# Optimization experiments

Measured on AMD Instinct MI355X. Metric: run time of the kernel, lower is better.

The kernel has to match this reference:

```python
import jax, jax.numpy as jnp
import numpy as np
from jax import lax

EPS = 1e-5
K = 3
PAD = 1
N_LAYERS = 7


def _conv2d(x, w, b):
    # x: [B,Cin,H,W], w: [Cout,Cin,K,K] -> [B,Cout,H,W], padding=1, stride=1
    y = lax.conv_general_dilated(x, w, window_strides=(1, 1),
                                 padding=[(PAD, PAD), (PAD, PAD)],
                                 dimension_numbers=('NCHW', 'OIHW', 'NCHW'))
    return y + b[None, :, None, None]


def _deform_conv2d(x, offset, weight):
    # torchvision deform_conv2d v1 (no mask, no bias), padding=PAD, stride=1.
    B, Cin, H, W = x.shape
    Cout = weight.shape[0]
    KK = K * K
    off = offset.reshape(B, KK, 2, H, W)
    dy = off[:, :, 0]  # [B,KK,H,W]
    dx = off[:, :, 1]
    kh = (jnp.arange(KK) // K).astype(x.dtype)  # row-major kernel taps
    kw = (jnp.arange(KK) % K).astype(x.dtype)
    hg = jnp.arange(H, dtype=x.dtype)
    wg = jnp.arange(W, dtype=x.dtype)
    # sampling positions p = p0 - pad + pk + offset
    py = dy + (hg[:, None] - PAD)[None, None, :, :] + kh[None, :, None, None]
    px = dx + (wg[None, :] - PAD)[None, None, :, :] + kw[None, :, None, None]
    y0 = jnp.floor(py)
    x0 = jnp.floor(px)
    ly = py - y0
    lx = px - x0
    y0i = y0.astype(jnp.int32)
    x0i = x0.astype(jnp.int32)

    def gather(img, yy, xx):  # img [Cin,H,W], yy/xx [KK,H,W]
        return img[:, yy, xx]  # [Cin,KK,H,W]

    gather_b = jax.vmap(gather)

    def corner(yi, xi, wgt):
        valid = (yi >= 0) & (yi < H) & (xi >= 0) & (xi < W)
        yc = jnp.clip(yi, 0, H - 1)
        xc = jnp.clip(xi, 0, W - 1)
        vals = gather_b(x, yc, xc)  # [B,Cin,KK,H,W]
        return vals * (wgt * valid)[:, None]

    sampled = (corner(y0i, x0i, (1 - ly) * (1 - lx))
               + corner(y0i, x0i + 1, (1 - ly) * lx)
               + corner(y0i + 1, x0i, ly * (1 - lx))
               + corner(y0i + 1, x0i + 1, ly * lx))  # [B,Cin,KK,H,W]
    return jnp.einsum('bikhw,oik->bohw', sampled, weight.reshape(Cout, Cin, KK))


def _layer(x, ow, ob, dw, g, b):
    offset = _conv2d(x, ow, ob)
    y = _deform_conv2d(x, offset, dw)
    # BatchNorm2d, training mode (batch stats, biased variance)
    mean = y.mean(axis=(0, 2, 3))
    var = y.var(axis=(0, 2, 3))
    yn = (y - mean[None, :, None, None]) * lax.rsqrt(var + EPS)[None, :, None, None]
    return jax.nn.relu(g[None, :, None, None] * yn + b[None, :, None, None])


def setup_inputs() -> dict:
    key = jax.random.key(0)
    ks = jax.random.split(key, 4)
    B, C, H, W = 4, 64, 128, 128
    x = jax.random.normal(ks[0], (B, C, H, W), dtype=jnp.float32)
    offset_w = jax.random.normal(ks[1], (N_LAYERS, 2 * K * K, C, K, K), dtype=jnp.float32) * 0.02
    offset_b = jnp.zeros((N_LAYERS, 2 * K * K), dtype=jnp.float32)
    deform_w = jax.random.normal(ks[2], (N_LAYERS, C, C, K, K), dtype=jnp.float32) * 0.05
    gamma = jnp.ones((N_LAYERS, C), dtype=jnp.float32)
    beta = jnp.zeros((N_LAYERS, C), dtype=jnp.float32)
    return {"x": x, "offset_w": offset_w, "offset_b": offset_b,
            "deform_w": deform_w, "gamma": gamma, "beta": beta}


def reference(x, offset_w, offset_b, deform_w, gamma, beta):
    def L(i, t):
        return _layer(t, offset_w[i], offset_b[i], deform_w[i], gamma[i], beta[i])
    # layer index map: 0=1_1, 1=1_2, 2=1_3, 3=1_4, 4=2_1, 5=2_2, 6=3
    out_1 = L(1, L(0, x))
    out_2 = L(4, x)
    out_sum_1 = out_1 + out_2
    out_1 = L(3, L(2, out_sum_1))
    out_2 = L(5, out_sum_1)
    out_3 = L(6, out_sum_1)
    return out_1 + out_2 + out_3
```

## Files before the change

### kernel.cpp

```cpp
#include <hip/hip_runtime.h>
#include <hip/hip_bf16.h>
#include <hip/hip_fp16.h>

#define NTOT 4194304
typedef __attribute__((ext_vector_type(4)))  short short4v;
typedef __attribute__((ext_vector_type(8)))  short short8v;
typedef __attribute__((ext_vector_type(4)))  float f32x4;
typedef __attribute__((ext_vector_type(2)))  float fx2;
typedef __attribute__((ext_vector_type(4)))  unsigned int uint4v;

__device__ __forceinline__ ushort f2bf(float f){
    __hip_bfloat16 h = __float2bfloat16(f);
    return __bfloat16_as_ushort(h);
}
__device__ __forceinline__ float bf2f(ushort u){
    return __uint_as_float(((unsigned)u)<<16);
}

__global__ __launch_bounds__(256) void pack_w(
    const float* __restrict__ dw, const float* __restrict__ ow,
    ushort* __restrict__ dwPk, ushort* __restrict__ owPk,
    float* __restrict__ statsG)
{
    int i = blockIdx.x*256 + threadIdx.x;
    if (i < 286720) {
        int j = i&3, co = (i>>2)&63, jg=(i>>8)&1, cih=(i>>9)&1, koff=(i>>10)&1;
        int r = i>>11; int kkp = r%5; int r2 = r/5; int ciq = r2&3; int l = r2>>2;
        int kk = kkp*2+koff, ci = ciq*16 + cih*8 + jg*4 + j;
        float v = (kk<9)? dw[((l*64+co)*64+ci)*9+kk] : 0.f;
        dwPk[i] = f2bf(v);
    }
    if (i < 143360) {
        int j = i&3, co = (i>>2)&31, jg=(i>>7)&1, cih=(i>>8)&1, koff=(i>>9)&1;
        int r = i>>10; int kkp = r%5; int r2 = r/5; int ciq = r2&3; int l = r2>>2;
        int kk = kkp*2+koff, ci = ciq*16 + cih*8 + jg*4 + j;
        float v = (kk<9 && co<18)? ow[((l*18+co)*64+ci)*9+kk] : 0.f;
        owPk[i] = f2bf(v);
    }
    if (i < 7*1024) statsG[i] = 0.f;
}

__global__ __launch_bounds__(256) void transpose_x(
    const float* __restrict__ src, ushort* __restrict__ xT)
{
    __shared__ ushort lds[128*72];
    const int bid = blockIdx.x, t = threadIdx.x;
    const int b = bid>>7, y = bid&127;
    const float* sp = src + (b<<20) + (y<<7);
#pragma unroll
    for (int i=0;i<32;i++){
        int lin = i*256 + t;
        int ci = lin>>7, xx = lin&127;
        lds[xx*72 + ci] = f2bf(sp[(ci<<14) + xx]);
    }
    __syncthreads();
    ushort* dp = xT + (((b<<7)+y)<<13);
#pragma unroll
    for (int i=0;i<4;i++){
        int u = i*256 + t;
        int xx = u>>3, cg = u&7;
        short8v v8 = *(const short8v*)(lds + xx*72 + cg*8);
        *(short8v*)(dp + (xx<<6) + cg*8) = v8;
    }
}

__constant__ int KHt[10] = {0,0,0,1,1,1,2,2,2,2};
__constant__ int KWt[10] = {0,1,2,0,1,2,0,1,2,2};

__global__ __attribute__((amdgpu_flat_work_group_size(512,512), amdgpu_waves_per_eu(4,8)))
void dcn_layer(
    const ushort* __restrict__ xTA, const ushort* __restrict__ xTB,
    const ushort* __restrict__ owPkB, const float* __restrict__ obB,
    const ushort* __restrict__ dwPkB, ushort* __restrict__ ybB,
    float* __restrict__ statsB, int l0, int l1)
{
    __shared__ __align__(16) char smem[79360];
    __half* offh = (__half*)(smem + 69120);

    const int t = threadIdx.x, lane = t&63, w = t>>6;
    const int l15 = lane&15, lg = lane>>4;
    const int cih = lg&1, koff = lane>>5;
    const int bid = blockIdx.x;
    const int lsel = bid >> 8;
    const int tb = bid & 255;
    const int L = lsel ? l1 : l0;
    const ushort* owPk = owPkB + L*20480;
    const float*  ob   = obB   + L*18;
    const ushort* dwPk = dwPkB + L*40960;
    ushort* yb         = ybB + (size_t)lsel*NTOT;
    float*  statsL     = statsB + L*1024;

    const int xcd = tb&7, idx = tb>>3;
    const int b = xcd>>1, vh = xcd&1;
    const int ht = vh*8 + (idx>>2), wt = idx&3;
    const int w0 = wt*32, h0 = ht*8;
    const int row = h0 + w;
    const int RLO = h0-5, CLO = w0-8;
    const ushort* xb = (lsel ? xTB : xTA) + (b<<20);

    const short8v zz8 = (short8v){0,0,0,0,0,0,0,0};
    auto stage = [&](int P){
#pragma unroll 1
        for (int i=0;i<7;i++){
            int d = i*512 + t;
            if (d < 3456) {
                int slot = d&3, sp = d>>2;
                int rowt = sp/48, colt = sp - rowt*48;
                int gy = RLO+rowt, gx = CLO+colt;
                bool ok = ((unsigned)gy<128u) && ((unsigned)gx<128u);
                int gyc = min(max(gy,0),127), gxc = min(max(gx,0),127);
                short8v v = *(const short8v*)(xb + (((gyc<<7)+gxc)<<6) + (P*4+slot)*8);
                if (!ok) v = zz8;
                *(short8v*)(smem + sp*80 + ((slot^(sp&3))<<4)) = v;
            }
        }
    };

    f32x4 oacc[2][2];
#pragma unroll
    for (int p=0;p<2;p++)
#pragma unroll
        for (int q=0;q<2;q++) oacc[p][q] = (f32x4){0.f,0.f,0.f,0.f};

#pragma unroll 1
    for (int P=0; P<2; ++P) {
        if (P) __syncthreads();
        stage(P);
        __syncthreads();
#pragma unroll 1
        for (int cil=0; cil<2; ++cil) {
            int ciq = P*2 + cil;
            int unit = (cil<<1)|cih;
#pragma unroll 1
            for (int kkp=0; kkp<5; ++kkp) {
                int kkA = 2*kkp;
                int kkB = (kkA+1>8)?8:(kkA+1);
                int kh = koff ? KHt[kkB] : KHt[kkA];
                int kw = koff ? KWt[kkB] : KWt[kkA];
                short8v afr[2];
#pragma unroll
                for (int p=0;p<2;p++){
                    int rowt = w + kh + 4;
                    int colt = p*16 + l15 + kw + 7;
                    int sp = rowt*48 + colt;
                    afr[p] = *(const short8v*)(smem + sp*80 + ((unit^(sp&3))<<4));
                }
                const ushort* wop = owPk + ciq*5120 + kkp*1024 + koff*512 + cih*256;
#pragma unroll
                for (int q=0;q<2;q++){
                    short4v b0 = *(const short4v*)(wop +       (q*16+l15)*4);
                    short4v b1 = *(const short4v*)(wop + 128 + (q*16+l15)*4);
                    short8v bb = __builtin_shufflevector(b0,b1,0,1,2,3,4,5,6,7);
#pragma unroll
                    for (int p=0;p<2;p++)
                        oacc[p][q] = __builtin_amdgcn_mfma_f32_16x16x32_bf16(afr[p], bb, oacc[p][q], 0,0,0);
                }
            }
        }
    }

    {
        float biasq[2];
#pragma unroll
        for (int q=0;q<2;q++){ int o = q*16+l15; biasq[q] = (o<18)? ob[o] : 0.f; }
#pragma unroll
        for (int p=0;p<2;p++)
#pragma unroll
            for (int q=0;q<2;q++){
                int o = q*16+l15;
                if (o < 18) {
#pragma unroll
                    for (int r=0;r<4;r++){
                        int pix = w*32 + p*16 + lg*4 + r;
                        offh[pix*20 + o] = __float2half(oacc[p][q][r] + biasq[q]);
                    }
                }
            }
    }

    f32x4 acc[2][4];
#pragma unroll
    for (int p=0;p<2;p++)
#pragma unroll
        for (int q=0;q<4;q++) acc[p][q] = (f32x4){0.f,0.f,0.f,0.f};

#pragma unroll 1
    for (int P=0; P<2; ++P) {
        __syncthreads();
        stage(P);
        __syncthreads();
#pragma unroll 1
        for (int cil=0; cil<2; ++cil) {
            int ciq = P*2 + cil;
            int unit = (cil<<1)|cih;
#pragma unroll 1
            for (int kkp=0; kkp<5; ++kkp) {
                int kkA = 2*kkp;
                int kkB = (kkA+1>8)?8:(kkA+1);
                int kh = koff ? KHt[kkB] : KHt[kkA];
                int kw = koff ? KWt[kkB] : KWt[kkA];
                int kkX = koff ? kkB : kkA;
                short8v afr[2];
#pragma unroll
                for (int p=0;p<2;p++){
                    int pix = w*32 + p*16 + l15;
                    unsigned odp = *(const unsigned*)((const char*)offh + pix*40 + 4*kkX);
                    float dy = __half2float(__ushort_as_half((ushort)(odp & 0xffffu)));
                    float dx = __half2float(__ushort_as_half((ushort)(odp >> 16)));
                    float py = (float)(row + kh - 1) + dy;
                    float px = (float)(w0 + p*16 + l15 + kw - 1) + dx;
                    float fy = floorf(py), fx = floorf(px);
                    float ly = py - fy, lx = px - fx;
                    int y0 = (int)fy, x0 = (int)fx;
                    int r0 = y0 - RLO, c0 = x0 - CLO;
                    int r1 = r0 + 1,  c1 = c0 + 1;
                    bool ty0 = ((unsigned)r0<18u), ty1 = ((unsigned)r1<18u);
                    bool tx0 = ((unsigned)c0<48u), tx1 = ((unsigned)c1<48u);
                    float w00 = (1.f-ly)*(1.f-lx), w01 = (1.f-ly)*lx;
                    float w10 = ly*(1.f-lx),       w11 = ly*lx;
                    float f00 = (ty0&&tx0)? w00 : 0.f;
                    float f01 = (ty0&&tx1)? w01 : 0.f;
                    float f10 = (ty1&&tx0)? w10 : 0.f;
                    float f11 = (ty1&&tx1)? w11 : 0.f;
                    int rc0 = min(max(r0,0),17), rc1 = min(max(r1,0),17);
                    int xc0 = min(max(c0,0),47), xc1 = min(max(c1,0),47);
                    int s00 = rc0*48+xc0, s01 = rc0*48+xc1, s10 = rc1*48+xc0, s11 = rc1*48+xc1;
                    uint4v q00 = *(const uint4v*)(smem + s00*80 + ((unit^(s00&3))<<4));
                    uint4v q01 = *(const uint4v*)(smem + s01*80 + ((unit^(s01&3))<<4));
                    uint4v q10 = *(const uint4v*)(smem + s10*80 + ((unit^(s10&3))<<4));
                    uint4v q11 = *(const uint4v*)(smem + s11*80 + ((unit^(s11&3))<<4));
                    fx2 F00 = {f00,f00}, F01 = {f01,f01}, F10 = {f10,f10}, F11 = {f11,f11};
                    fx2 sv2[4];
#pragma unroll
                    for (int k=0;k<4;k++){
                        fx2 xa = {__uint_as_float(q00[k]<<16), __uint_as_float(q00[k]&0xffff0000u)};
                        fx2 xb2= {__uint_as_float(q01[k]<<16), __uint_as_float(q01[k]&0xffff0000u)};
                        fx2 xc = {__uint_as_float(q10[k]<<16), __uint_as_float(q10[k]&0xffff0000u)};
                        fx2 xd = {__uint_as_float(q11[k]<<16), __uint_as_float(q11[k]&0xffff0000u)};
                        sv2[k] = xa*F00 + xb2*F01 + xc*F10 + xd*F11;
                    }
                    bool allIn = ty0 && ty1 && tx0 && tx1;
                    bool inY = (y0 >= -1) && (y0 <= 127);
                    bool inX = (x0 >= -1) && (x0 <= 127);
                    if (__builtin_expect(!allIn && inY && inX, 0)) {
                        bool vy0 = ((unsigned)y0<128u), vy1 = ((unsigned)(y0+1)<128u);
                        bool vx0 = ((unsigned)x0<128u), vx1 = ((unsigned)(x0+1)<128u);
                        float rw00 = (vy0&&vx0&&!(ty0&&tx0))? w00 : 0.f;
                        float rw01 = (vy0&&vx1&&!(ty0&&tx1))? w01 : 0.f;
                        float rw10 = (vy1&&vx0&&!(ty1&&tx0))? w10 : 0.f;
                        float rw11 = (vy1&&vx1&&!(ty1&&tx1))? w11 : 0.f;
                        int y0c=min(max(y0,0),127), y1c=min(max(y0+1,0),127);
                        int x0c=min(max(x0,0),127), x1c=min(max(x0+1,0),127);
                        int cofs = (ciq*2 + cih)*8;
                        short8v a0 = *(const short8v*)(xb + ((((y0c<<7)+x0c)<<6) + cofs));
                        short8v a1 = *(const short8v*)(xb + ((((y0c<<7)+x1c)<<6) + cofs));
                        short8v a2 = *(const short8v*)(xb + ((((y1c<<7)+x0c)<<6) + cofs));
                        short8v a3 = *(const short8v*)(xb + ((((y1c<<7)+x1c)<<6) + cofs));
#pragma unroll
                        for (int j=0;j<8;j++){
                            float add = rw00*bf2f((ushort)a0[j]) + rw01*bf2f((ushort)a1[j])
                                      + rw10*bf2f((ushort)a2[j]) + rw11*bf2f((ushort)a3[j]);
                            if (j&1) sv2[j>>1].y += add; else sv2[j>>1].x += add;
                        }
                    }
#pragma unroll
                    for (int k=0;k<4;k++){
                        afr[p][2*k]   = (short)f2bf(sv2[k].x);
                        afr[p][2*k+1] = (short)f2bf(sv2[k].y);
                    }
                }
                const ushort* wp = dwPk + ciq*10240 + kkp*2048 + koff*1024 + cih*512;
#pragma unroll
                for (int q=0;q<4;q++){
                    short4v b0 = *(const short4v*)(wp +       (q*16+l15)*4);
                    short4v b1 = *(const short4v*)(wp + 256 + (q*16+l15)*4);
                    short8v bb = __builtin_shufflevector(b0,b1,0,1,2,3,4,5,6,7);
                    acc[0][q] = __builtin_amdgcn_mfma_f32_16x16x32_bf16(afr[0], bb, acc[0][q], 0,0,0);
                    acc[1][q] = __builtin_amdgcn_mfma_f32_16x16x32_bf16(afr[1], bb, acc[1][q], 0,0,0);
                }
            }
        }
    }

    float* yt  = (float*)smem;
    float* red = (float*)(smem + 33280);
#pragma unroll
    for (int half=0; half<2; ++half){
        __syncthreads();
#pragma unroll
        for (int p=0;p<2;p++)
#pragma unroll
            for (int qq=0;qq<2;qq++)
                *(f32x4*)(yt + (qq*16+l15)*260 + w*32 + p*16 + lg*4) = acc[p][half*2+qq];
        __syncthreads();
#pragma unroll
        for (int i=0;i<2;i++){
            int u = i*512 + t;
            int co = u>>5, px8 = (u&31)*8;
            short8v v8;
#pragma unroll
            for (int e=0;e<8;e++) v8[e] = (short)f2bf(yt[co*260 + px8 + e]);
            *(short8v*)(yb + ((((b<<6) + half*32 + co)<<14)
                        + ((h0 + (px8>>5))<<7) + w0 + (px8&31))) = v8;
        }
        {
            float s=0.f, s2=0.f;
            int co = t&31, seg = t>>5;
            const float* bp = yt + co*260 + seg*16;
#pragma unroll
            for (int qd=0;qd<16;qd++){ float v = bp[qd]; s += v; s2 += v*v; }
            red[seg*32+co] = s; red[512 + seg*32+co] = s2;
        }
        __syncthreads();
        if (t < 64){
            int vv = t>>5, cc = t&31;
            float a = 0.f;
#pragma unroll
            for (int g=0;g<16;g++) a += red[vv*512 + g*32 + cc];
            atomicAdd(statsL + (tb&7)*128 + vv*64 + half*32 + cc, a);
        }
    }
}

__global__ __launch_bounds__(256) void norm_fuse(
    const ushort* __restrict__ yv, const float* __restrict__ statsL,
    const float* __restrict__ gamma, const float* __restrict__ beta,
    const ushort* __restrict__ addB, float* __restrict__ dstF,
    ushort* __restrict__ dstB, ushort* __restrict__ xTout, int mode)
{
    __shared__ float scs[64], shs[64];
    __shared__ ushort lt[128*72];
    const int bid = blockIdx.x, t = threadIdx.x;
    const int b = bid>>7, y = bid&127;
    if (t < 64){
        float sum=0.f, ssq=0.f;
#pragma unroll
        for (int s=0;s<8;s++){ sum += statsL[s*128+t]; ssq += statsL[s*128+64+t]; }
        float mean = sum*(1.f/65536.f);
        float var  = ssq*(1.f/65536.f) - mean*mean;
        float inv  = rsqrtf(var + 1e-5f);
        float sc = gamma[t]*inv;
        scs[t] = sc; shs[t] = beta[t] - mean*sc;
    }
    __syncthreads();
#pragma unroll
    for (int i=0;i<4;i++){
        int g = i*256 + t;
        int ch = g>>4, xg = (g&15)*8;
        long base = (long)(((b<<6)+ch)<<14) + (y<<7) + xg;
        short8v v8 = *(const short8v*)(yv + base);
        float sc = scs[ch], sh = shs[ch];
        float r[8];
#pragma unroll
        for (int e=0;e<8;e++) r[e] = fmaxf(bf2f((ushort)v8[e])*sc+sh, 0.f);
        if (mode & 2) {
            short8v a8 = *(const short8v*)(addB + base);
#pragma unroll
            for (int e=0;e<8;e++) r[e] += bf2f((ushort)a8[e]);
        }
        if (mode & 4) {
            const float4* op = (const float4*)(dstF + base);
            float4 a0 = op[0], a1 = op[1];
            r[0]+=a0.x; r[1]+=a0.y; r[2]+=a0.z; r[3]+=a0.w;
            r[4]+=a1.x; r[5]+=a1.y; r[6]+=a1.z; r[7]+=a1.w;
        }
        if (mode & 5) {
            float4* dp = (float4*)(dstF + base);
            dp[0] = make_float4(r[0],r[1],r[2],r[3]);
            dp[1] = make_float4(r[4],r[5],r[6],r[7]);
        }
        if (mode & 16) {
            short8v o8;
#pragma unroll
            for (int e=0;e<8;e++) o8[e] = (short)f2bf(r[e]);
            *(short8v*)(dstB + base) = o8;
        }
        if (mode & 8) {
#pragma unroll
            for (int e=0;e<8;e++) lt[(xg+e)*72 + ch] = f2bf(r[e]);
        }
    }
    if (mode & 8) {
        __syncthreads();
        ushort* dp = xTout + (((b<<7)+y)<<13);
#pragma unroll
        for (int i=0;i<4;i++){
            int u = i*256 + t;
            int xx = u>>3, cg = u&7;
            short8v v8 = *(const short8v*)(lt + xx*72 + cg*8);
            *(short8v*)(dp + (xx<<6) + cg*8) = v8;
        }
    }
}

extern "C" void kernel_launch(void* const* d_in, const int* in_sizes, int n_in,
                              void* d_out, int out_size, void* d_ws, size_t ws_size,
                              hipStream_t stream)
{
    const float* x  = (const float*)d_in[0];
    const float* ow = (const float*)d_in[1];
    const float* ob = (const float*)d_in[2];
    const float* dw = (const float*)d_in[3];
    const float* g  = (const float*)d_in[4];
    const float* be = (const float*)d_in[5];
    float* out = (float*)d_out;

    ushort* yb     = (ushort*)d_ws;
    ushort* t4b    = yb + 2*(size_t)NTOT;
    ushort* xA     = t4b + NTOT;
    ushort* xB     = xA + NTOT;
    float*  statsG = (float*)(xB + NTOT);
    ushort* dwPk   = (ushort*)(statsG + 7*1024);
    ushort* owPk   = dwPk + 286720;

    pack_w<<<1120, 256, 0, stream>>>(dw, ow, dwPk, owPk, statsG);
    transpose_x<<<512, 256, 0, stream>>>(x, xA);

    auto nf = [&](int l, const ushort* ybp, int mode, const ushort* addB,
                  float* dstF, ushort* dstB, ushort* xout){
        norm_fuse<<<512, 256, 0, stream>>>(ybp, statsG + l*1024, g + l*64, be + l*64,
                                           addB, dstF, dstB, xout, mode);
    };

    dcn_layer<<<512, 512, 0, stream>>>(xA, xA, owPk, ob, dwPk, yb, statsG, 4, 0);
    nf(4, yb,        16, nullptr, nullptr, t4b,    nullptr);
    nf(0, yb+NTOT,    8, nullptr, nullptr, nullptr, xB);
    dcn_layer<<<256, 512, 0, stream>>>(xB, xB, owPk, ob, dwPk, yb, statsG, 1, 1);
    nf(1, yb,        10, t4b,    nullptr, nullptr, xA);
    dcn_layer<<<512, 512, 0, stream>>>(xA, xA, owPk, ob, dwPk, yb, statsG, 2, 5);
    nf(2, yb,         8, nullptr, nullptr, nullptr, xB);
    nf(5, yb+NTOT,    1, nullptr, out,     nullptr, nullptr);
    dcn_layer<<<512, 512, 0, stream>>>(xB, xA, owPk, ob, dwPk, yb, statsG, 3, 6);
    nf(3, yb,         5, nullptr, out,     nullptr, nullptr);
    nf(6, yb+NTOT,    5, nullptr, out,     nullptr, nullptr);
}
```

Baseline: 295.4 us.

## Fuse final three BN+ReLU passes and hoist per-tap sampling math out of channel loop

Swaps the loop order in both conv phases so the tap loop is outer and the channel-half loop is unrolled inside. Offset decoding, bilinear weights and LDS addresses are then computed once per tap and reused for both channel halves. Layer 5's output now goes to a separate buffer and layer 6's into t4b, so a new norm3 kernel normalizes layers 3, 5 and 6 in one pass and writes the output once. This removes three read-modify-write passes over the fp32 output, at the cost of higher register pressure from the hoisted per-pixel arrays.

Result: faster. 270.4 us (-8.5%).

```diff
diff --git a/kernel.cpp b/kernel.cpp
--- a/kernel.cpp
+++ b/kernel.cpp
@@ -71,8 +71,8 @@
 void dcn_layer(
     const ushort* __restrict__ xTA, const ushort* __restrict__ xTB,
     const ushort* __restrict__ owPkB, const float* __restrict__ obB,
-    const ushort* __restrict__ dwPkB, ushort* __restrict__ ybB,
-    float* __restrict__ statsB, int l0, int l1)
+    const ushort* __restrict__ dwPkB, ushort* __restrict__ ybA,
+    ushort* __restrict__ ybX, float* __restrict__ statsB, int l0, int l1)
 {
     __shared__ __align__(16) char smem[79360];
     __half* offh = (__half*)(smem + 69120);
@@ -87,7 +87,7 @@
     const ushort* owPk = owPkB + L*20480;
     const float*  ob   = obB   + L*18;
     const ushort* dwPk = dwPkB + L*40960;
-    ushort* yb         = ybB + (size_t)lsel*NTOT;
+    ushort* yb         = lsel ? ybX : ybA;
     float*  statsL     = statsB + L*1024;
 
     const int xcd = tb&7, idx = tb>>3;
@@ -128,24 +128,25 @@
         stage(P);
         __syncthreads();
 #pragma unroll 1
-        for (int cil=0; cil<2; ++cil) {
-            int ciq = P*2 + cil;
-            int unit = (cil<<1)|cih;
-#pragma unroll 1
-            for (int kkp=0; kkp<5; ++kkp) {
-                int kkA = 2*kkp;
-                int kkB = (kkA+1>8)?8:(kkA+1);
-                int kh = koff ? KHt[kkB] : KHt[kkA];
-                int kw = koff ? KWt[kkB] : KWt[kkA];
+        for (int kkp=0; kkp<5; ++kkp) {
+            int kkA = 2*kkp;
+            int kkB2 = (kkA+1>8)?8:(kkA+1);
+            int kh = koff ? KHt[kkB2] : KHt[kkA];
+            int kw = koff ? KWt[kkB2] : KWt[kkA];
+            int PC[2], M4[2];
+#pragma unroll
+            for (int p=0;p<2;p++){
+                int sp = (w + kh + 4)*48 + (p*16 + l15 + kw + 7);
+                PC[p] = sp*80; M4[p] = (sp&3)<<4;
+            }
+#pragma unroll
+            for (int cil=0; cil<2; ++cil) {
+                int u4 = (((cil<<1)|cih)<<4);
                 short8v afr[2];
 #pragma unroll
-                for (int p=0;p<2;p++){
-                    int rowt = w + kh + 4;
-                    int colt = p*16 + l15 + kw + 7;
-                    int sp = rowt*48 + colt;
-                    afr[p] = *(const short8v*)(smem + sp*80 + ((unit^(sp&3))<<4));
-                }
-                const ushort* wop = owPk + ciq*5120 + kkp*1024 + koff*512 + cih*256;
+                for (int p=0;p<2;p++)
+                    afr[p] = *(const short8v*)(smem + PC[p] + (u4 ^ M4[p]));
+                const ushort* wop = owPk + (P*2+cil)*5120 + kkp*1024 + koff*512 + cih*256;
 #pragma unroll
                 for (int q=0;q<2;q++){
                     short4v b0 = *(const short4v*)(wop +       (q*16+l15)*4);
@@ -190,46 +191,59 @@
         stage(P);
         __syncthreads();
 #pragma unroll 1
-        for (int cil=0; cil<2; ++cil) {
-            int ciq = P*2 + cil;
-            int unit = (cil<<1)|cih;
-#pragma unroll 1
-            for (int kkp=0; kkp<5; ++kkp) {
-                int kkA = 2*kkp;
-                int kkB = (kkA+1>8)?8:(kkA+1);
-                int kh = koff ? KHt[kkB] : KHt[kkA];
-                int kw = koff ? KWt[kkB] : KWt[kkA];
-                int kkX = koff ? kkB : kkA;
+        for (int kkp=0; kkp<5; ++kkp) {
+            int kkA = 2*kkp;
+            int kkB2 = (kkA+1>8)?8:(kkA+1);
+            int kh = koff ? KHt[kkB2] : KHt[kkA];
+            int kw = koff ? KWt[kkB2] : KWt[kkA];
+            int kkX = koff ? kkB2 : kkA;
+            float F00[2],F01[2],F10[2],F11[2];
+            int PC0[2],PC1[2],PC2[2],PC3[2], M40[2],M41[2],M42[2],M43[2];
+            bool FB[2];
+#pragma unroll
+            for (int p=0;p<2;p++){
+                int pix = w*32 + p*16 + l15;
+                unsigned odp = *(const unsigned*)((const char*)offh + pix*40 + 4*kkX);
+                float dy = __half2float(__ushort_as_half((ushort)(odp & 0xffffu)));
+                float dx = __half2float(__ushort_as_half((ushort)(odp >> 16)));
+                float py = (float)(row + kh - 1) + dy;
+                float px = (float)(w0 + p*16 + l15 + kw - 1) + dx;
+                float fy = floorf(py), fx = floorf(px);
+                float ly = py - fy, lx = px - fx;
+                int y0 = (int)fy, x0 = (int)fx;
+                int r0 = y0 - RLO, c0 = x0 - CLO;
+                int r1 = r0 + 1,  c1 = c0 + 1;
+                bool ty0 = ((unsigned)r0<18u), ty1 = ((unsigned)r1<18u);
+                bool tx0 = ((unsigned)c0<48u), tx1 = ((unsigned)c1<48u);
+                float w00 = (1.f-ly)*(1.f-lx), w01 = (1.f-ly)*lx;
+                float w10 = ly*(1.f-lx),       w11 = ly*lx;
+                F00[p] = (ty0&&tx0)? w00 : 0.f;
+                F01[p] = (ty0&&tx1)? w01 : 0.f;
+                F10[p] = (ty1&&tx0)? w10 : 0.f;
+                F11[p] = (ty1&&tx1)? w11 : 0.f;
+                int rc0 = min(max(r0,0),17), rc1 = min(max(r1,0),17);
+                int xc0 = min(max(c0,0),47), xc1 = min(max(c1,0),47);
+                int s00 = rc0*48+xc0, s01 = rc0*48+xc1, s10 = rc1*48+xc0, s11 = rc1*48+xc1;
+                PC0[p]=s00*80; M40[p]=(s00&3)<<4;
+                PC1[p]=s01*80; M41[p]=(s01&3)<<4;
+                PC2[p]=s10*80; M42[p]=(s10&3)<<4;
+                PC3[p]=s11*80; M43[p]=(s11&3)<<4;
+                bool allIn = ty0 && ty1 && tx0 && tx1;
+                FB[p] = !allIn && (y0>=-1)&&(y0<=127)&&(x0>=-1)&&(x0<=127);
+            }
+#pragma unroll
+            for (int cil=0; cil<2; ++cil) {
+                int ciq = P*2 + cil;
+                int u4 = (((cil<<1)|cih)<<4);
                 short8v afr[2];
 #pragma unroll
                 for (int p=0;p<2;p++){
-                    int pix = w*32 + p*16 + l15;
-                    unsigned odp = *(const unsigned*)((const char*)offh + pix*40 + 4*kkX);
-                    float dy = __half2float(__ushort_as_half((ushort)(odp & 0xffffu)));
-                    float dx = __half2float(__ushort_as_half((ushort)(odp >> 16)));
-                    float py = (float)(row + kh - 1) + dy;
-                    float px = (float)(w0 + p*16 + l15 + kw - 1) + dx;
-                    float fy = floorf(py), fx = floorf(px);
-                    float ly = py - fy, lx = px - fx;
-                    int y0 = (int)fy, x0 = (int)fx;
-                    int r0 = y0 - RLO, c0 = x0 - CLO;
-                    int r1 = r0 + 1,  c1 = c0 + 1;
-                    bool ty0 = ((unsigned)r0<18u), ty1 = ((unsigned)r1<18u);
-                    bool tx0 = ((unsigned)c0<48u), tx1 = ((unsigned)c1<48u);
-                    float w00 = (1.f-ly)*(1.f-lx), w01 = (1.f-ly)*lx;
-                    float w10 = ly*(1.f-lx),       w11 = ly*lx;
-                    float f00 = (ty0&&tx0)? w00 : 0.f;
-                    float f01 = (ty0&&tx1)? w01 : 0.f;
-                    float f10 = (ty1&&tx0)? w10 : 0.f;
-                    float f11 = (ty1&&tx1)? w11 : 0.f;
-                    int rc0 = min(max(r0,0),17), rc1 = min(max(r1,0),17);
-                    int xc0 = min(max(c0,0),47), xc1 = min(max(c1,0),47);
-                    int s00 = rc0*48+xc0, s01 = rc0*48+xc1, s10 = rc1*48+xc0, s11 = rc1*48+xc1;
-                    uint4v q00 = *(const uint4v*)(smem + s00*80 + ((unit^(s00&3))<<4));
-                    uint4v q01 = *(const uint4v*)(smem + s01*80 + ((unit^(s01&3))<<4));
-                    uint4v q10 = *(const uint4v*)(smem + s10*80 + ((unit^(s10&3))<<4));
-                    uint4v q11 = *(const uint4v*)(smem + s11*80 + ((unit^(s11&3))<<4));
-                    fx2 F00 = {f00,f00}, F01 = {f01,f01}, F10 = {f10,f10}, F11 = {f11,f11};
+                    uint4v q00 = *(const uint4v*)(smem + PC0[p] + (u4^M40[p]));
+                    uint4v q01 = *(const uint4v*)(smem + PC1[p] + (u4^M41[p]));
+                    uint4v q10 = *(const uint4v*)(smem + PC2[p] + (u4^M42[p]));
+                    uint4v q11 = *(const uint4v*)(smem + PC3[p] + (u4^M43[p]));
+                    fx2 Fa = {F00[p],F00[p]}, Fb = {F01[p],F01[p]};
+                    fx2 Fc = {F10[p],F10[p]}, Fd = {F11[p],F11[p]};
                     fx2 sv2[4];
 #pragma unroll
                     for (int k=0;k<4;k++){
@@ -237,14 +251,25 @@
                         fx2 xb2= {__uint_as_float(q01[k]<<16), __uint_as_float(q01[k]&0xffff0000u)};
                         fx2 xc = {__uint_as_float(q10[k]<<16), __uint_as_float(q10[k]&0xffff0000u)};
                         fx2 xd = {__uint_as_float(q11[k]<<16), __uint_as_float(q11[k]&0xffff0000u)};
-                        sv2[k] = xa*F00 + xb2*F01 + xc*F10 + xd*F11;
+                        sv2[k] = xa*Fa + xb2*Fb + xc*Fc + xd*Fd;
                     }
-                    bool allIn = ty0 && ty1 && tx0 && tx1;
-                    bool inY = (y0 >= -1) && (y0 <= 127);
-                    bool inX = (x0 >= -1) && (x0 <= 127);
-                    if (__builtin_expect(!allIn && inY && inX, 0)) {
+                    if (__builtin_expect(FB[p], 0)) {
+                        int pix = w*32 + p*16 + l15;
+                        unsigned odp = *(const unsigned*)((const char*)offh + pix*40 + 4*kkX);
+                        float dy = __half2float(__ushort_as_half((ushort)(odp & 0xffffu)));
+                        float dx = __half2float(__ushort_as_half((ushort)(odp >> 16)));
+                        float py = (float)(row + kh - 1) + dy;
+                        float px = (float)(w0 + p*16 + l15 + kw - 1) + dx;
+                        float fy = floorf(py), fx = floorf(px);
+                        float ly = py - fy, lx = px - fx;
+                        int y0 = (int)fy, x0 = (int)fx;
+                        int r0 = y0 - RLO, c0 = x0 - CLO;
+                        bool ty0 = ((unsigned)r0<18u), ty1 = ((unsigned)(r0+1)<18u);
+                        bool tx0 = ((unsigned)c0<48u), tx1 = ((unsigned)(c0+1)<48u);
                         bool vy0 = ((unsigned)y0<128u), vy1 = ((unsigned)(y0+1)<128u);
                         bool vx0 = ((unsigned)x0<128u), vx1 = ((unsigned)(x0+1)<128u);
+                        float w00 = (1.f-ly)*(1.f-lx), w01 = (1.f-ly)*lx;
+                        float w10 = ly*(1.f-lx),       w11 = ly*lx;
                         float rw00 = (vy0&&vx0&&!(ty0&&tx0))? w00 : 0.f;
                         float rw01 = (vy0&&vx1&&!(ty0&&tx1))? w01 : 0.f;
                         float rw10 = (vy1&&vx0&&!(ty1&&tx0))? w10 : 0.f;
@@ -393,6 +418,52 @@
     }
 }
 
+__global__ __launch_bounds__(256) void norm3(
+    const ushort* __restrict__ ya, const ushort* __restrict__ ybp,
+    const ushort* __restrict__ yc, const float* __restrict__ statsG,
+    const float* __restrict__ gamma, const float* __restrict__ beta,
+    int la, int lb, int lc, float* __restrict__ out)
+{
+    __shared__ float sc3[3][64], sh3[3][64];
+    const int bid = blockIdx.x, t = threadIdx.x;
+    const int b = bid>>7, y = bid&127;
+    if (t < 192){
+        int set = t>>6, ch = t&63;
+        int l = (set==0)? la : ((set==1)? lb : lc);
+        const float* st = statsG + l*1024;
+        float sum=0.f, ssq=0.f;
+#pragma unroll
+        for (int s=0;s<8;s++){ sum += st[s*128+ch]; ssq += st[s*128+64+ch]; }
+        float mean = sum*(1.f/65536.f);
+        float var  = ssq*(1.f/65536.f) - mean*mean;
+        float inv  = rsqrtf(var + 1e-5f);
+        float sc = gamma[l*64+ch]*inv;
+        sc3[set][ch] = sc; sh3[set][ch] = beta[l*64+ch] - mean*sc;
+    }
+    __syncthreads();
+#pragma unroll
+    for (int i=0;i<4;i++){
+        int g = i*256 + t;
+        int ch = g>>4, xg = (g&15)*8;
+        long base = (long)(((b<<6)+ch)<<14) + (y<<7) + xg;
+        short8v a8 = *(const short8v*)(ya  + base);
+        short8v b8 = *(const short8v*)(ybp + base);
+        short8v c8 = *(const short8v*)(yc  + base);
+        float sa = sc3[0][ch], ha = sh3[0][ch];
+        float sb = sc3[1][ch], hb = sh3[1][ch];
+        float sc = sc3[2][ch], hc = sh3[2][ch];
+        float r[8];
+#pragma unroll
+        for (int e=0;e<8;e++)
+            r[e] = fmaxf(bf2f((ushort)a8[e])*sa+ha, 0.f)
+                 + fmaxf(bf2f((ushort)b8[e])*sb+hb, 0.f)
+                 + fmaxf(bf2f((ushort)c8[e])*sc+hc, 0.f);
+        float4* dp = (float4*)(out + base);
+        dp[0] = make_float4(r[0],r[1],r[2],r[3]);
+        dp[1] = make_float4(r[4],r[5],r[6],r[7]);
+    }
+}
+
 extern "C" void kernel_launch(void* const* d_in, const int* in_sizes, int n_in,
                               void* d_out, int out_size, void* d_ws, size_t ws_size,
                               hipStream_t stream)
@@ -405,8 +476,9 @@
     const float* be = (const float*)d_in[5];
     float* out = (float*)d_out;
 
-    ushort* yb     = (ushort*)d_ws;
-    ushort* t4b    = yb + 2*(size_t)NTOT;
+    ushort* yb0    = (ushort*)d_ws;
+    ushort* yb1    = yb0 + NTOT;
+    ushort* t4b    = yb1 + NTOT;
     ushort* xA     = t4b + NTOT;
     ushort* xB     = xA + NTOT;
     float*  statsG = (float*)(xB + NTOT);
@@ -422,15 +494,13 @@
                                            addB, dstF, dstB, xout, mode);
     };
 
-    dcn_layer<<<512, 512, 0, stream>>>(xA, xA, owPk, ob, dwPk, yb, statsG, 4, 0);
-    nf(4, yb,        16, nullptr, nullptr, t4b,    nullptr);
-    nf(0, yb+NTOT,    8, nullptr, nullptr, nullptr, xB);
-    dcn_layer<<<256, 512, 0, stream>>>(xB, xB, owPk, ob, dwPk, yb, statsG, 1, 1);
-    nf(1, yb,        10, t4b,    nullptr, nullptr, xA);
-    dcn_layer<<<512, 512, 0, stream>>>(xA, xA, owPk, ob, dwPk, yb, statsG, 2, 5);
-    nf(2, yb,         8, nullptr, nullptr, nullptr, xB);
-    nf(5, yb+NTOT,    1, nullptr, out,     nullptr, nullptr);
-    dcn_layer<<<512, 512, 0, stream>>>(xB, xA, owPk, ob, dwPk, yb, statsG, 3, 6);
-    nf(3, yb,         5, nullptr, out,     nullptr, nullptr);
-    nf(6, yb+NTOT,    5, nullptr, out,     nullptr, nullptr);
-}
+    dcn_layer<<<512, 512, 0, stream>>>(xA, xA, owPk, ob, dwPk, yb0, yb1, statsG, 4, 0);
+    nf(4, yb0,       16, nullptr, nullptr, t4b,    nullptr);
+    nf(0, yb1,        8, nullptr, nullptr, nullptr, xB);
+    dcn_layer<<<256, 512, 0, stream>>>(xB, xB, owPk, ob, dwPk, yb0, yb0, statsG, 1, 1);
+    nf(1, yb0,       10, t4b,    nullptr, nullptr, xA);
+    dcn_layer<<<512, 512, 0, stream>>>(xA, xA, owPk, ob, dwPk, yb0, yb1, statsG, 2, 5);
+    nf(2, yb0,        8, nullptr, nullptr, nullptr, xB);
+    dcn_layer<<<512, 512, 0, stream>>>(xB, xA, owPk, ob, dwPk, yb0, t4b, statsG, 3, 6);
+    norm3<<<512, 256, 0, stream>>>(yb0, yb1, t4b, statsG, g, be, 3, 5, 6, out);
+}
```
